# Performance work log

Hardware: AMD Instinct MI355X
Metric: run time of the kernel (lower is better)

## Reference

```python
import jax, jax.numpy as jnp
import numpy as np

D_MODEL = 1024
N_HEADS = 16
D_K = 64

def setup_inputs() -> dict:
    key = jax.random.key(0)
    k0, k1, k2, k3, k4 = jax.random.split(key, 5)
    B, S = 4, 4096
    std = 0.02
    x = jax.random.normal(k0, (B, S, D_MODEL), dtype=jnp.float32)
    # nn.Linear weights are [out, in]; init normal(0, 0.02) as in _init_weights
    W_q = std * jax.random.normal(k1, (N_HEADS * D_K, D_MODEL), dtype=jnp.float32)
    W_k = std * jax.random.normal(k2, (N_HEADS * D_K, D_MODEL), dtype=jnp.float32)
    W_v = std * jax.random.normal(k3, (N_HEADS * D_K, D_MODEL), dtype=jnp.float32)
    W_o = std * jax.random.normal(k4, (D_MODEL, N_HEADS * D_K), dtype=jnp.float32)
    return {"x": x, "W_q": W_q, "W_k": W_k, "W_v": W_v, "W_o": W_o}

def reference(x, W_q, W_k, W_v, W_o):
    B, S, _ = x.shape
    H, Dk = N_HEADS, D_K
    # projections (nn.Linear: x @ W.T), reshape to [B, S, H, Dk]
    q = (x @ W_q.T).reshape(B, S, H, Dk)
    k = (x @ W_k.T).reshape(B, S, H, Dk)
    v = (x @ W_v.T).reshape(B, S, H, Dk)
    scale = 1.0 / jnp.sqrt(jnp.float32(Dk))
    # No softmax between the two matmuls -> reassociate (QK^T)V = Q(K^TV),
    # identical math, O(S*d^2) instead of O(S^2*d).
    kv = jnp.einsum('bshd,bshe->bhde', k, v)          # [B, H, Dk, Dk]
    attn = jnp.einsum('bshd,bhde->bshe', q, kv) * scale  # [B, S, H, Dk]
    out = attn.reshape(B, S, H * Dk) @ W_o.T
    return out
```

## Files before the change

kernel.cpp:

```cpp
#include <hip/hip_runtime.h>
#include <hip/hip_bf16.h>
#include <cstdint>


typedef __bf16 bf16x8 __attribute__((ext_vector_type(8)));
typedef float f32x4 __attribute__((ext_vector_type(4)));
typedef unsigned short ushort_t;

__device__ inline void gld_lds16(const void* g, void* l) {
    __builtin_amdgcn_global_load_lds(
        (const __attribute__((address_space(1))) unsigned int*)g,
        (__attribute__((address_space(3))) unsigned int*)l,
        16, 0, 0);
}

__device__ inline ushort_t f2bf(float f) {
    uint32_t u = __float_as_uint(f);
    uint32_t r = (u + 0x7fffu + ((u >> 16) & 1u)) >> 16;
    return (ushort_t)r;
}
__device__ inline float bf2f(ushort_t u) {
    return __uint_as_float((uint32_t)u << 16);
}

template <typename OutT>
__global__ __launch_bounds__(256, 2)
void gemm_bt(const ushort_t* __restrict__ A, int lda, long strideA,
             const ushort_t* __restrict__ B, int ldb, long strideB,
             OutT* __restrict__ C0, int ldc0, long strideC0, int K)
{
    __shared__ ushort_t lA[128 * 32];
    __shared__ ushort_t lB[128 * 32];

    const int t    = threadIdx.x;
    const int lane = t & 63;
    const int wid  = t >> 6;
    const int z    = blockIdx.z;

    A += (size_t)z * strideA;
    B += (size_t)z * strideB;

    const int m0 = blockIdx.x * 128;
    const int n0 = blockIdx.y * 128;

    const int wm = (wid >> 1) * 64;
    const int wn = (wid & 1) * 64;
    const int mr = lane & 15;
    const int q4 = lane >> 4;

    const int row_a = t >> 2;
    const int seg   = ((t & 3) ^ ((t >> 3) & 3)) * 8;
    const int csw   = (q4 ^ ((mr >> 1) & 3)) * 16;

    f32x4 acc[4][4] = {};

    for (int k0 = 0; k0 < K; k0 += 32) {
        __syncthreads();
        gld_lds16(A + (size_t)(m0 + row_a) * lda + k0 + seg,      (char*)lA + wid * 1024);
        gld_lds16(A + (size_t)(m0 + 64 + row_a) * lda + k0 + seg, (char*)lA + 4096 + wid * 1024);
        gld_lds16(B + (size_t)(n0 + row_a) * ldb + k0 + seg,      (char*)lB + wid * 1024);
        gld_lds16(B + (size_t)(n0 + 64 + row_a) * ldb + k0 + seg, (char*)lB + 4096 + wid * 1024);
        __syncthreads();

        bf16x8 af[4], bf[4];
#pragma unroll
        for (int i = 0; i < 4; ++i)
            af[i] = *(const bf16x8*)((const char*)lA + (wm + i * 16 + mr) * 64 + csw);
#pragma unroll
        for (int j = 0; j < 4; ++j)
            bf[j] = *(const bf16x8*)((const char*)lB + (wn + j * 16 + mr) * 64 + csw);
#pragma unroll
        for (int i = 0; i < 4; ++i)
#pragma unroll
            for (int j = 0; j < 4; ++j)
                acc[i][j] = __builtin_amdgcn_mfma_f32_16x16x32_bf16(af[i], bf[j], acc[i][j], 0, 0, 0);
    }

    OutT* Cw = C0 + (size_t)z * strideC0;
#pragma unroll
    for (int i = 0; i < 4; ++i) {
        const int rbase = m0 + wm + i * 16 + q4 * 4;
#pragma unroll
        for (int j = 0; j < 4; ++j) {
            const int col = n0 + wn + j * 16 + mr;
#pragma unroll
            for (int r = 0; r < 4; ++r) {
                const float v = acc[i][j][r];
                const size_t off = (size_t)(rbase + r) * ldc0 + col;
                if constexpr (sizeof(OutT) == 2) Cw[off] = f2bf(v);
                else                             Cw[off] = v;
            }
        }
    }
}

__global__ __launch_bounds__(256, 2)
void gemm_gram(const ushort_t* __restrict__ X, ushort_t* __restrict__ Gp)
{
    __shared__ ushort_t lA[128 * 32];
    __shared__ ushort_t lB[128 * 32];

    const int t    = threadIdx.x;
    const int lane = t & 63;
    const int wid  = t >> 6;

    const int z  = blockIdx.x;
    const int bb = z >> 2, ks = z & 3;

    int ti = 0, rem = blockIdx.y;
    while (rem >= 8 - ti) { rem -= 8 - ti; ++ti; }
    const int tj = ti + rem;
    const int m0 = ti * 128;
    const int n0 = tj * 128;

    const ushort_t* A = X + (size_t)bb * 4096 + (size_t)ks * 1024;

    const int wm = (wid >> 1) * 64;
    const int wn = (wid & 1) * 64;
    const int mr = lane & 15;
    const int q4 = lane >> 4;

    const int row_a = t >> 2;
    const int seg   = ((t & 3) ^ ((t >> 3) & 3)) * 8;
    const int csw   = (q4 ^ ((mr >> 1) & 3)) * 16;

    f32x4 acc[4][4] = {};

    for (int k0 = 0; k0 < 1024; k0 += 32) {
        __syncthreads();
        gld_lds16(A + (size_t)(m0 + row_a) * 16384 + k0 + seg,      (char*)lA + wid * 1024);
        gld_lds16(A + (size_t)(m0 + 64 + row_a) * 16384 + k0 + seg, (char*)lA + 4096 + wid * 1024);
        gld_lds16(A + (size_t)(n0 + row_a) * 16384 + k0 + seg,      (char*)lB + wid * 1024);
        gld_lds16(A + (size_t)(n0 + 64 + row_a) * 16384 + k0 + seg, (char*)lB + 4096 + wid * 1024);
        __syncthreads();

        bf16x8 af[4], bf[4];
#pragma unroll
        for (int i = 0; i < 4; ++i)
            af[i] = *(const bf16x8*)((const char*)lA + (wm + i * 16 + mr) * 64 + csw);
#pragma unroll
        for (int j = 0; j < 4; ++j)
            bf[j] = *(const bf16x8*)((const char*)lB + (wn + j * 16 + mr) * 64 + csw);
#pragma unroll
        for (int i = 0; i < 4; ++i)
#pragma unroll
            for (int j = 0; j < 4; ++j)
                acc[i][j] = __builtin_amdgcn_mfma_f32_16x16x32_bf16(af[i], bf[j], acc[i][j], 0, 0, 0);
    }

    ushort_t* Cw = Gp + ((size_t)z << 20);
#pragma unroll
    for (int i = 0; i < 4; ++i) {
        const int rbase = m0 + wm + i * 16 + q4 * 4;
#pragma unroll
        for (int j = 0; j < 4; ++j) {
            const int col = n0 + wn + j * 16 + mr;
#pragma unroll
            for (int r = 0; r < 4; ++r)
                Cw[(size_t)(rbase + r) * 1024 + col] = f2bf(acc[i][j][r]);
        }
    }
}

__global__ __launch_bounds__(256)
void reduce_g_t(const ushort_t* __restrict__ Gp, ushort_t* __restrict__ G)
{
    __shared__ float acc[64 * 65];

    const int t  = threadIdx.x;
    const int b  = blockIdx.y;
    const int tr = blockIdx.x >> 4, tc = blockIdx.x & 15;
    const int sr = (tr <= tc) ? tr : tc;
    const int sc = (tr <= tc) ? tc : tr;
    const bool flip = tr > tc;

#pragma unroll
    for (int p = 0; p < 4; ++p) {
        const int idx = p * 256 + t;
        const int r = idx >> 4, c = (idx & 15) * 4;
        float a0 = 0.f, a1 = 0.f, a2 = 0.f, a3 = 0.f;
#pragma unroll
        for (int ksl = 0; ksl < 4; ++ksl) {
            const ushort4 u = *(const ushort4*)&Gp[((size_t)(b * 4 + ksl) << 20)
                                                   + (size_t)(sr * 64 + r) * 1024 + sc * 64 + c];
            a0 += bf2f(u.x); a1 += bf2f(u.y); a2 += bf2f(u.z); a3 += bf2f(u.w);
        }
        acc[r * 65 + c + 0] = a0;
        acc[r * 65 + c + 1] = a1;
        acc[r * 65 + c + 2] = a2;
        acc[r * 65 + c + 3] = a3;
    }
    __syncthreads();

#pragma unroll
    for (int p = 0; p < 4; ++p) {
        const int idx = p * 256 + t;
        const int r = idx >> 4, c = (idx & 15) * 4;
        float v0, v1, v2, v3;
        if (flip) {
            v0 = acc[(c + 0) * 65 + r];
            v1 = acc[(c + 1) * 65 + r];
            v2 = acc[(c + 2) * 65 + r];
            v3 = acc[(c + 3) * 65 + r];
        } else {
            v0 = acc[r * 65 + c + 0];
            v1 = acc[r * 65 + c + 1];
            v2 = acc[r * 65 + c + 2];
            v3 = acc[r * 65 + c + 3];
        }
        ushort4 o;
        o.x = f2bf(v0); o.y = f2bf(v1); o.z = f2bf(v2); o.w = f2bf(v3);
        *(ushort4*)&G[((size_t)b << 20) + (size_t)(tr * 64 + r) * 1024 + tc * 64 + c] = o;
    }
}

__global__ __launch_bounds__(256)
void cast_x_t(const float* __restrict__ x, ushort_t* __restrict__ xb,
              ushort_t* __restrict__ xbT)
{
    __shared__ ushort_t lt[64 * 66];
    const int t  = threadIdx.x;
    const int s0 = blockIdx.x * 64;
    const int i0 = blockIdx.y * 64;

#pragma unroll
    for (int c = 0; c < 4; ++c) {
        const int idx = c * 256 + t;
        const int r = idx >> 4, c4 = (idx & 15) * 4;
        const float4 f = *(const float4*)&x[(size_t)(s0 + r) * 1024 + i0 + c4];
        ushort4 o;
        o.x = f2bf(f.x); o.y = f2bf(f.y); o.z = f2bf(f.z); o.w = f2bf(f.w);
        *(ushort4*)&xb[(size_t)(s0 + r) * 1024 + i0 + c4] = o;
        *(uint32_t*)&lt[r * 66 + c4]     = (uint32_t)o.x | ((uint32_t)o.y << 16);
        *(uint32_t*)&lt[r * 66 + c4 + 2] = (uint32_t)o.z | ((uint32_t)o.w << 16);
    }
    __syncthreads();
#pragma unroll
    for (int c = 0; c < 4; ++c) {
        const int idx = c * 256 + t;
        const int ri = idx >> 4, s4 = (idx & 15) * 4;
        ushort4 o;
        o.x = lt[(s4 + 0) * 66 + ri];
        o.y = lt[(s4 + 1) * 66 + ri];
        o.z = lt[(s4 + 2) * 66 + ri];
        o.w = lt[(s4 + 3) * 66 + ri];
        *(ushort4*)&xbT[(size_t)(i0 + ri) * 16384 + s0 + s4] = o;
    }
}

__global__ __launch_bounds__(256)
void cast_wt(const float* __restrict__ W, ushort_t* __restrict__ WT)
{
    __shared__ ushort_t lt[64 * 66];
    const int t  = threadIdx.x;
    const int r0 = blockIdx.x * 64;
    const int c0 = blockIdx.y * 64;

#pragma unroll
    for (int c = 0; c < 4; ++c) {
        const int idx = c * 256 + t;
        const int r = idx >> 4, c4 = (idx & 15) * 4;
        const float4 f = *(const float4*)&W[(size_t)(r0 + r) * 1024 + c0 + c4];
        ushort4 o;
        o.x = f2bf(f.x); o.y = f2bf(f.y); o.z = f2bf(f.z); o.w = f2bf(f.w);
        *(uint32_t*)&lt[r * 66 + c4]     = (uint32_t)o.x | ((uint32_t)o.y << 16);
        *(uint32_t*)&lt[r * 66 + c4 + 2] = (uint32_t)o.z | ((uint32_t)o.w << 16);
    }
    __syncthreads();
#pragma unroll
    for (int c = 0; c < 4; ++c) {
        const int idx = c * 256 + t;
        const int ri = idx >> 4, s4 = (idx & 15) * 4;
        ushort4 o;
        o.x = lt[(s4 + 0) * 66 + ri];
        o.y = lt[(s4 + 1) * 66 + ri];
        o.z = lt[(s4 + 2) * 66 + ri];
        o.w = lt[(s4 + 3) * 66 + ri];
        *(ushort4*)&WT[(size_t)(c0 + ri) * 1024 + r0 + s4] = o;
    }
}

__global__ __launch_bounds__(256)
void cast_w2(const float* __restrict__ a, const float* __restrict__ b,
             ushort_t* __restrict__ out)
{
    const float* src = (blockIdx.y == 0) ? a : b;
    const int i = (blockIdx.x * 256 + threadIdx.x) * 4;
    const float4 f = *(const float4*)&src[i];
    ushort4 o;
    o.x = f2bf(f.x); o.y = f2bf(f.y); o.z = f2bf(f.z); o.w = f2bf(f.w);
    *(ushort4*)&out[(size_t)blockIdx.y * 1048576 + i] = o;
}

__global__ __launch_bounds__(256)
void kvblk(const ushort_t* __restrict__ H, const ushort_t* __restrict__ Wv,
           float* __restrict__ KVp)
{
    __shared__ ushort_t sH[64 * 132];
    __shared__ ushort_t sV[64 * 132];

    const int t  = threadIdx.x;
    const int is = blockIdx.x;
    const int bh = blockIdx.y;
    const int b  = bh >> 4, h = bh & 15;

    const ushort_t* Hp = H + ((size_t)b << 20) + (size_t)(h * 64) * 1024 + is * 128;
    const ushort_t* Vp = Wv + (size_t)(h * 64) * 1024 + is * 128;

#pragma unroll
    for (int i2 = 0; i2 < 8; ++i2) {
        const int ci = i2 * 256 + t;
        const int r = ci >> 5, c = (ci & 31) * 4;
        *(uint2*)&sH[r * 132 + c] = *(const uint2*)&Hp[(size_t)r * 1024 + c];
        *(uint2*)&sV[r * 132 + c] = *(const uint2*)&Vp[(size_t)r * 1024 + c];
    }
    __syncthreads();

    const int d0 = (t >> 4) * 4;
    const int e0 = (t & 15) * 4;
    float acc[4][4] = {};

#pragma unroll 2
    for (int i4 = 0; i4 < 128; i4 += 4) {
        uint2 hu[4], vu[4];
#pragma unroll
        for (int j = 0; j < 4; ++j) {
            hu[j] = *(const uint2*)&sH[(d0 + j) * 132 + i4];
            vu[j] = *(const uint2*)&sV[(e0 + j) * 132 + i4];
        }
        float hf[4][4], vf[4][4];
#pragma unroll
        for (int j = 0; j < 4; ++j) {
            hf[j][0] = __uint_as_float(hu[j].x << 16);
            hf[j][1] = __uint_as_float(hu[j].x & 0xffff0000u);
            hf[j][2] = __uint_as_float(hu[j].y << 16);
            hf[j][3] = __uint_as_float(hu[j].y & 0xffff0000u);
            vf[j][0] = __uint_as_float(vu[j].x << 16);
            vf[j][1] = __uint_as_float(vu[j].x & 0xffff0000u);
            vf[j][2] = __uint_as_float(vu[j].y << 16);
            vf[j][3] = __uint_as_float(vu[j].y & 0xffff0000u);
        }
#pragma unroll
        for (int ii = 0; ii < 4; ++ii)
#pragma unroll
            for (int di = 0; di < 4; ++di)
#pragma unroll
                for (int ej = 0; ej < 4; ++ej)
                    acc[di][ej] += hf[di][ii] * vf[ej][ii];
    }

    float* outp = KVp + ((size_t)(is * 64 + bh)) * 4096;
#pragma unroll
    for (int i = 0; i < 4; ++i) {
        float4 o; o.x = acc[i][0]; o.y = acc[i][1]; o.z = acc[i][2]; o.w = acc[i][3];
        *(float4*)&outp[(d0 + i) * 64 + e0] = o;
    }
}

__global__ __launch_bounds__(256)
void reduce_kv8(const float4* __restrict__ in, float4* __restrict__ out)
{
    const int i = blockIdx.x * 256 + threadIdx.x;
    float4 a = in[i];
#pragma unroll
    for (int s = 1; s < 8; ++s) {
        const float4 b = in[s * 65536 + i];
        a.x += b.x; a.y += b.y; a.z += b.z; a.w += b.w;
    }
    out[i] = a;
}

__global__ __launch_bounds__(256)
void make_E(const float* __restrict__ KV, const float* __restrict__ Wo,
            ushort_t* __restrict__ Et)
{
    __shared__ float skv[64 * 65];
    __shared__ float swo[64 * 65];

    const int t  = threadIdx.x;
    const int bh = blockIdx.y;
    const int b  = bh >> 4, h = bh & 15;
    const int j0 = blockIdx.x * 64;

    const float* kvp = KV + (size_t)bh * 4096;
#pragma unroll
    for (int i = 0; i < 4; ++i) {
        const int idx = t + i * 256;
        const int r = idx >> 4, c = (idx & 15) * 4;
        const float4 f = *(const float4*)&kvp[r * 64 + c];
        skv[r * 65 + c + 0] = f.x;
        skv[r * 65 + c + 1] = f.y;
        skv[r * 65 + c + 2] = f.z;
        skv[r * 65 + c + 3] = f.w;
        const float4 g = *(const float4*)&Wo[(size_t)(j0 + r) * 1024 + h * 64 + c];
        swo[r * 65 + c + 0] = g.x;
        swo[r * 65 + c + 1] = g.y;
        swo[r * 65 + c + 2] = g.z;
        swo[r * 65 + c + 3] = g.w;
    }
    __syncthreads();

    const int d0 = (t & 15) * 4;
#pragma unroll
    for (int pass = 0; pass < 4; ++pass) {
        const int jloc = (t >> 4) + pass * 16;
        float s0 = 0.f, s1 = 0.f, s2 = 0.f, s3 = 0.f;
        const float* wrow = &swo[jloc * 65];
#pragma unroll 8
        for (int e = 0; e < 64; ++e) {
            const float w = wrow[e];
            s0 += skv[(d0 + 0) * 65 + e] * w;
            s1 += skv[(d0 + 1) * 65 + e] * w;
            s2 += skv[(d0 + 2) * 65 + e] * w;
            s3 += skv[(d0 + 3) * 65 + e] * w;
        }
        ushort4 o;
        o.x = f2bf(s0 * 0.125f);
        o.y = f2bf(s1 * 0.125f);
        o.z = f2bf(s2 * 0.125f);
        o.w = f2bf(s3 * 0.125f);
        *(ushort4*)&Et[((size_t)b * 1024 + j0 + jloc) * 1024 + h * 64 + d0] = o;
    }
}


extern "C" void kernel_launch(void* const* d_in, const int* in_sizes, int n_in,
                              void* d_out, int out_size, void* d_ws, size_t ws_size,
                              hipStream_t stream)
{
    const float* x  = (const float*)d_in[0];
    const float* Wq = (const float*)d_in[1];
    const float* Wk = (const float*)d_in[2];
    const float* Wv = (const float*)d_in[3];
    const float* Wo = (const float*)d_in[4];
    float* out = (float*)d_out;

    const int B = 4, S = 4096, D = 1024;
    const long MB1 = 1048576;

    char* ws = (char*)d_ws;
    size_t off = 0;
    auto alloc = [&](size_t bytes) -> void* {
        void* p = ws + off;
        off += (bytes + 255) & ~(size_t)255;
        return p;
    };
    ushort_t* xb   = (ushort_t*)alloc((size_t)B * S * D * 2);
    ushort_t* xbT  = (ushort_t*)alloc((size_t)D * B * S * 2);
    ushort_t* wkv  = (ushort_t*)alloc((size_t)2 * D * D * 2);
    ushort_t* wqT  = (ushort_t*)alloc((size_t)D * D * 2);
    ushort_t* Gb   = (ushort_t*)alloc((size_t)B * D * D * 2);
    float*    kvp  = (float*)alloc((size_t)8 * 64 * 4096 * 4);
    float*    kvr  = (float*)alloc((size_t)64 * 4096 * 4);
    ushort_t* Fb   = (ushort_t*)alloc((size_t)B * D * D * 2);
    char*     R1   = (char*)alloc((size_t)16 * MB1 * 2);
    ushort_t* Gp = (ushort_t*)R1;
    ushort_t* Hb = (ushort_t*)R1;
    ushort_t* Et = (ushort_t*)(R1 + 8 * MB1 * 2);
    ushort_t* wkb = wkv;
    ushort_t* wvb = wkv + MB1;

    cast_x_t<<<dim3(256, 16), dim3(256), 0, stream>>>(x, xb, xbT);
    cast_w2<<<dim3(1024, 2), dim3(256), 0, stream>>>(Wk, Wv, wkv);
    cast_wt<<<dim3(16, 16), dim3(256), 0, stream>>>(Wq, wqT);

    gemm_gram<<<dim3(16, 36), dim3(256), 0, stream>>>(xbT, Gp);
    reduce_g_t<<<dim3(256, 4), dim3(256), 0, stream>>>(Gp, Gb);

    gemm_bt<ushort_t><<<dim3(8, 8, 4), dim3(256), 0, stream>>>(
        wkb, D, 0, Gb, D, MB1, Hb, D, MB1, D);

    kvblk<<<dim3(8, 64), dim3(256), 0, stream>>>(Hb, wvb, kvp);
    reduce_kv8<<<dim3(256), dim3(256), 0, stream>>>((const float4*)kvp, (float4*)kvr);

    make_E<<<dim3(16, 64), dim3(256), 0, stream>>>(kvr, Wo, Et);

    gemm_bt<ushort_t><<<dim3(8, 8, 4), dim3(256), 0, stream>>>(
        Et, D, MB1, wqT, D, 0, Fb, D, (long)D * D, D);

    gemm_bt<float><<<dim3(32, 8, 4), dim3(256), 0, stream>>>(
        xb, D, (long)S * D, Fb, D, (long)D * D, out, D, (long)S * D, D);
}
```

Baseline: 315.9 us.

## Add pipelined 256x256 GEMM, narrower mid GEMMs, fused weight casts, atomic KV reduce

The final x·F GEMM now uses a new 256x256-tile, 512-thread kernel with a 4-stage LDS ring buffer, explicit waitcnt/barrier scheduling and MFMA priority boosts, to raise data reuse and overlap loads with compute. The two 1024x1024 batched GEMMs switch to a 128x64 tile variant so more blocks fill the device. The weight casts merge into one launch that also zeroes the KV buffer, and the per-split KV partials are accumulated with float atomics instead of a separate reduction kernel. In exchange, the atomic summation order is nondeterministic and the large GEMM uses 128KB of LDS, which limits occupancy.

```diff
diff --git a/kernel.cpp b/kernel.cpp
--- a/kernel.cpp
+++ b/kernel.cpp
@@ -24,13 +24,13 @@
 }
 
 template <typename OutT>
-__global__ __launch_bounds__(256, 2)
-void gemm_bt(const ushort_t* __restrict__ A, int lda, long strideA,
-             const ushort_t* __restrict__ B, int ldb, long strideB,
-             OutT* __restrict__ C0, int ldc0, long strideC0, int K)
+__global__ __launch_bounds__(256, 4)
+void gemm_bt_n64(const ushort_t* __restrict__ A, int lda, long strideA,
+                 const ushort_t* __restrict__ B, int ldb, long strideB,
+                 OutT* __restrict__ C0, int ldc0, long strideC0, int K)
 {
     __shared__ ushort_t lA[128 * 32];
-    __shared__ ushort_t lB[128 * 32];
+    __shared__ ushort_t lB[64 * 32];
 
     const int t    = threadIdx.x;
     const int lane = t & 63;
@@ -41,10 +41,10 @@
     B += (size_t)z * strideB;
 
     const int m0 = blockIdx.x * 128;
-    const int n0 = blockIdx.y * 128;
+    const int n0 = blockIdx.y * 64;
 
     const int wm = (wid >> 1) * 64;
-    const int wn = (wid & 1) * 64;
+    const int wn = (wid & 1) * 32;
     const int mr = lane & 15;
     const int q4 = lane >> 4;
 
@@ -52,27 +52,26 @@
     const int seg   = ((t & 3) ^ ((t >> 3) & 3)) * 8;
     const int csw   = (q4 ^ ((mr >> 1) & 3)) * 16;
 
-    f32x4 acc[4][4] = {};
+    f32x4 acc[4][2] = {};
 
     for (int k0 = 0; k0 < K; k0 += 32) {
         __syncthreads();
         gld_lds16(A + (size_t)(m0 + row_a) * lda + k0 + seg,      (char*)lA + wid * 1024);
         gld_lds16(A + (size_t)(m0 + 64 + row_a) * lda + k0 + seg, (char*)lA + 4096 + wid * 1024);
         gld_lds16(B + (size_t)(n0 + row_a) * ldb + k0 + seg,      (char*)lB + wid * 1024);
-        gld_lds16(B + (size_t)(n0 + 64 + row_a) * ldb + k0 + seg, (char*)lB + 4096 + wid * 1024);
         __syncthreads();
 
-        bf16x8 af[4], bf[4];
+        bf16x8 af[4], bf[2];
 #pragma unroll
         for (int i = 0; i < 4; ++i)
             af[i] = *(const bf16x8*)((const char*)lA + (wm + i * 16 + mr) * 64 + csw);
 #pragma unroll
-        for (int j = 0; j < 4; ++j)
+        for (int j = 0; j < 2; ++j)
             bf[j] = *(const bf16x8*)((const char*)lB + (wn + j * 16 + mr) * 64 + csw);
 #pragma unroll
         for (int i = 0; i < 4; ++i)
 #pragma unroll
-            for (int j = 0; j < 4; ++j)
+            for (int j = 0; j < 2; ++j)
                 acc[i][j] = __builtin_amdgcn_mfma_f32_16x16x32_bf16(af[i], bf[j], acc[i][j], 0, 0, 0);
     }
 
@@ -81,7 +80,7 @@
     for (int i = 0; i < 4; ++i) {
         const int rbase = m0 + wm + i * 16 + q4 * 4;
 #pragma unroll
-        for (int j = 0; j < 4; ++j) {
+        for (int j = 0; j < 2; ++j) {
             const int col = n0 + wn + j * 16 + mr;
 #pragma unroll
             for (int r = 0; r < 4; ++r) {
@@ -90,6 +89,121 @@
                 if constexpr (sizeof(OutT) == 2) Cw[off] = f2bf(v);
                 else                             Cw[off] = v;
             }
+        }
+    }
+}
+
+__global__ __launch_bounds__(512, 2)
+void gemm256_bt(const ushort_t* __restrict__ A, int lda, long strideA,
+                const ushort_t* __restrict__ B, int ldb, long strideB,
+                float* __restrict__ C, int ldc, long strideC, int K)
+{
+    __shared__ char lds[131072];
+
+    const int t    = threadIdx.x;
+    const int lane = t & 63;
+    const int wid  = t >> 6;
+    const int z    = blockIdx.z;
+
+    A += (size_t)z * strideA;
+    B += (size_t)z * strideB;
+
+    const int m0 = blockIdx.x * 256;
+    const int n0 = blockIdx.y * 256;
+
+    const int wm = wid >> 2;
+    const int wn = wid & 3;
+    const int mr = lane & 15;
+    const int q4 = lane >> 4;
+
+    const int NT = K >> 5;
+
+    const int srow = t >> 2;
+    const int scol = (t & 3) * 8;
+
+    auto stage = [&](const ushort_t* __restrict__ src, int ld, int org,
+                     int tgt, int boff) {
+        if (tgt >= NT) return;
+        char* base = lds + ((tgt & 3) << 15) + boff + wid * 1024;
+        const ushort_t* g = src + (size_t)(org + srow) * ld + tgt * 32 + scol;
+        gld_lds16(g, base);
+        gld_lds16(g + ((size_t)ld << 7), base + 8192);
+    };
+
+    bf16x8 aX[4], aY[4], bB[4];
+
+    auto rdA4 = [&](bf16x8 (&dst)[4], const char* bufA, int half) {
+#pragma unroll
+        for (int i = 0; i < 4; ++i) {
+            const int row = wm * 128 + (half * 4 + i) * 16 + mr;
+            dst[i] = *(const bf16x8*)(bufA + row * 64 + q4 * 16);
+        }
+    };
+    auto rdB4 = [&](const char* bufB) {
+#pragma unroll
+        for (int j = 0; j < 4; ++j) {
+            const int row = wn * 64 + j * 16 + mr;
+            bB[j] = *(const bf16x8*)(bufB + row * 64 + q4 * 16);
+        }
+    };
+
+    f32x4 acc[8][4] = {};
+    auto MM = [&](int half, bf16x8 (&a)[4]) {
+        __builtin_amdgcn_s_setprio(1);
+#pragma unroll
+        for (int i = 0; i < 4; ++i)
+#pragma unroll
+            for (int j = 0; j < 4; ++j)
+                acc[half * 4 + i][j] = __builtin_amdgcn_mfma_f32_16x16x32_bf16(
+                    a[i], bB[j], acc[half * 4 + i][j], 0, 0, 0);
+        __builtin_amdgcn_s_setprio(0);
+    };
+
+#define BAR()   __builtin_amdgcn_s_barrier()
+#define SB()    __builtin_amdgcn_sched_barrier(0)
+#define LGKM0() asm volatile("s_waitcnt lgkmcnt(0)" ::: "memory")
+
+    stage(A, lda, m0, 0, 0); stage(B, ldb, n0, 0, 16384);
+    stage(A, lda, m0, 1, 0); stage(B, ldb, n0, 1, 16384);
+    stage(A, lda, m0, 2, 0); stage(B, ldb, n0, 2, 16384);
+    asm volatile("s_waitcnt vmcnt(4)" ::: "memory");
+    BAR();
+    rdA4(aX, lds, 0); rdB4(lds + 16384); SB();
+
+    for (int kt = 0; kt < NT; ++kt) {
+        const char* bufC = lds + ((kt & 3) << 15);
+        const char* bufN = lds + (((kt + 1) & 3) << 15);
+
+        stage(B, ldb, n0, kt + 3, 16384);
+        BAR(); LGKM0(); SB();
+        rdA4(aY, bufC, 1); SB();
+        MM(0, aX); SB();
+        BAR();
+        stage(A, lda, m0, kt + 3, 0);
+        BAR(); LGKM0(); SB();
+        MM(1, aY); SB();
+        if (kt + 1 < NT) {
+            if (kt <= NT - 4) asm volatile("s_waitcnt vmcnt(4)" ::: "memory");
+            else              asm volatile("s_waitcnt vmcnt(0)" ::: "memory");
+            rdA4(aX, bufN, 0); rdB4(bufN + 16384); SB();
+        }
+        BAR();
+    }
+
+#undef BAR
+#undef SB
+#undef LGKM0
+
+    float* Cw = C + (size_t)z * strideC;
+#pragma unroll
+    for (int i = 0; i < 8; ++i) {
+        const int rbase = m0 + wm * 128 + i * 16 + q4 * 4;
+#pragma unroll
+        for (int j = 0; j < 4; ++j) {
+            const int col = n0 + wn * 64 + j * 16 + mr;
+#pragma unroll
+            for (int r = 0; r < 4; ++r)
+                Cw[(size_t)(rbase + r) * ldc + col] = acc[i][j][r];
         }
     }
 }
@@ -249,18 +363,39 @@
 }
 
 __global__ __launch_bounds__(256)
-void cast_wt(const float* __restrict__ W, ushort_t* __restrict__ WT)
+void cast_weights(const float* __restrict__ Wk, const float* __restrict__ Wv,
+                  const float* __restrict__ Wq, ushort_t* __restrict__ wkv,
+                  ushort_t* __restrict__ wqT, float* __restrict__ kvr)
 {
     __shared__ ushort_t lt[64 * 66];
     const int t  = threadIdx.x;
-    const int r0 = blockIdx.x * 64;
-    const int c0 = blockIdx.y * 64;
-
+    const int bx = blockIdx.x;
+    const int y  = blockIdx.y;
+
+    if (y < 2) {
+        const float* src = y ? Wv : Wk;
+        ushort_t* dst = wkv + (size_t)y * 1048576;
+#pragma unroll
+        for (int it = 0; it < 4; ++it) {
+            const int i = ((it * 256 + bx) * 256 + t) * 4;
+            const float4 f = *(const float4*)&src[i];
+            ushort4 o;
+            o.x = f2bf(f.x); o.y = f2bf(f.y); o.z = f2bf(f.z); o.w = f2bf(f.w);
+            *(ushort4*)&dst[i] = o;
+        }
+        return;
+    }
+
+    float4 zz; zz.x = 0.f; zz.y = 0.f; zz.z = 0.f; zz.w = 0.f;
+    *(float4*)&kvr[(size_t)(bx * 256 + t) * 4] = zz;
+
+    const int r0 = (bx >> 4) * 64;
+    const int c0 = (bx & 15) * 64;
 #pragma unroll
     for (int c = 0; c < 4; ++c) {
         const int idx = c * 256 + t;
         const int r = idx >> 4, c4 = (idx & 15) * 4;
-        const float4 f = *(const float4*)&W[(size_t)(r0 + r) * 1024 + c0 + c4];
+        const float4 f = *(const float4*)&Wq[(size_t)(r0 + r) * 1024 + c0 + c4];
         ushort4 o;
         o.x = f2bf(f.x); o.y = f2bf(f.y); o.z = f2bf(f.z); o.w = f2bf(f.w);
         *(uint32_t*)&lt[r * 66 + c4]     = (uint32_t)o.x | ((uint32_t)o.y << 16);
@@ -276,25 +411,13 @@
         o.y = lt[(s4 + 1) * 66 + ri];
         o.z = lt[(s4 + 2) * 66 + ri];
         o.w = lt[(s4 + 3) * 66 + ri];
-        *(ushort4*)&WT[(size_t)(c0 + ri) * 1024 + r0 + s4] = o;
-    }
-}
-
-__global__ __launch_bounds__(256)
-void cast_w2(const float* __restrict__ a, const float* __restrict__ b,
-             ushort_t* __restrict__ out)
-{
-    const float* src = (blockIdx.y == 0) ? a : b;
-    const int i = (blockIdx.x * 256 + threadIdx.x) * 4;
-    const float4 f = *(const float4*)&src[i];
-    ushort4 o;
-    o.x = f2bf(f.x); o.y = f2bf(f.y); o.z = f2bf(f.z); o.w = f2bf(f.w);
-    *(ushort4*)&out[(size_t)blockIdx.y * 1048576 + i] = o;
+        *(ushort4*)&wqT[(size_t)(c0 + ri) * 1024 + r0 + s4] = o;
+    }
 }
 
 __global__ __launch_bounds__(256)
 void kvblk(const ushort_t* __restrict__ H, const ushort_t* __restrict__ Wv,
-           float* __restrict__ KVp)
+           float* __restrict__ kvr)
 {
     __shared__ ushort_t sH[64 * 132];
     __shared__ ushort_t sV[64 * 132];
@@ -349,25 +472,12 @@
                     acc[di][ej] += hf[di][ii] * vf[ej][ii];
     }
 
-    float* outp = KVp + ((size_t)(is * 64 + bh)) * 4096;
-#pragma unroll
-    for (int i = 0; i < 4; ++i) {
-        float4 o; o.x = acc[i][0]; o.y = acc[i][1]; o.z = acc[i][2]; o.w = acc[i][3];
-        *(float4*)&outp[(d0 + i) * 64 + e0] = o;
-    }
-}
-
-__global__ __launch_bounds__(256)
-void reduce_kv8(const float4* __restrict__ in, float4* __restrict__ out)
-{
-    const int i = blockIdx.x * 256 + threadIdx.x;
-    float4 a = in[i];
-#pragma unroll
-    for (int s = 1; s < 8; ++s) {
-        const float4 b = in[s * 65536 + i];
-        a.x += b.x; a.y += b.y; a.z += b.z; a.w += b.w;
-    }
-    out[i] = a;
+    float* outp = kvr + (size_t)bh * 4096;
+#pragma unroll
+    for (int i = 0; i < 4; ++i)
+#pragma unroll
+        for (int j = 0; j < 4; ++j)
+            atomicAdd(&outp[(d0 + i) * 64 + e0 + j], acc[i][j]);
 }
 
 __global__ __launch_bounds__(256)
@@ -450,7 +560,6 @@
     ushort_t* wkv  = (ushort_t*)alloc((size_t)2 * D * D * 2);
     ushort_t* wqT  = (ushort_t*)alloc((size_t)D * D * 2);
     ushort_t* Gb   = (ushort_t*)alloc((size_t)B * D * D * 2);
-    float*    kvp  = (float*)alloc((size_t)8 * 64 * 4096 * 4);
     float*    kvr  = (float*)alloc((size_t)64 * 4096 * 4);
     ushort_t* Fb   = (ushort_t*)alloc((size_t)B * D * D * 2);
     char*     R1   = (char*)alloc((size_t)16 * MB1 * 2);
@@ -461,23 +570,21 @@
     ushort_t* wvb = wkv + MB1;
 
     cast_x_t<<<dim3(256, 16), dim3(256), 0, stream>>>(x, xb, xbT);
-    cast_w2<<<dim3(1024, 2), dim3(256), 0, stream>>>(Wk, Wv, wkv);
-    cast_wt<<<dim3(16, 16), dim3(256), 0, stream>>>(Wq, wqT);
+    cast_weights<<<dim3(256, 3), dim3(256), 0, stream>>>(Wk, Wv, Wq, wkv, wqT, kvr);
 
     gemm_gram<<<dim3(16, 36), dim3(256), 0, stream>>>(xbT, Gp);
     reduce_g_t<<<dim3(256, 4), dim3(256), 0, stream>>>(Gp, Gb);
 
-    gemm_bt<ushort_t><<<dim3(8, 8, 4), dim3(256), 0, stream>>>(
+    gemm_bt_n64<ushort_t><<<dim3(8, 16, 4), dim3(256), 0, stream>>>(
         wkb, D, 0, Gb, D, MB1, Hb, D, MB1, D);
 
-    kvblk<<<dim3(8, 64), dim3(256), 0, stream>>>(Hb, wvb, kvp);
-    reduce_kv8<<<dim3(256), dim3(256), 0, stream>>>((const float4*)kvp, (float4*)kvr);
+    kvblk<<<dim3(8, 64), dim3(256), 0, stream>>>(Hb, wvb, kvr);
 
     make_E<<<dim3(16, 64), dim3(256), 0, stream>>>(kvr, Wo, Et);
 
-    gemm_bt<ushort_t><<<dim3(8, 8, 4), dim3(256), 0, stream>>>(
+    gemm_bt_n64<ushort_t><<<dim3(8, 16, 4), dim3(256), 0, stream>>>(
         Et, D, MB1, wqT, D, 0, Fb, D, (long)D * D, D);
 
-    gemm_bt<float><<<dim3(32, 8, 4), dim3(256), 0, stream>>>(
+    gemm256_bt<<<dim3(16, 4, 4), dim3(512), 0, stream>>>(
         xb, D, (long)S * D, Fb, D, (long)D * D, out, D, (long)S * D, D);
 }
```

Result: slower. 324.5 us (+2.7%).
